# Kernel tuning notes

Measured on AMD Instinct MI355X. Metric: run time of the kernel, lower is better.

The kernel has to match this reference:

```python
import jax, jax.numpy as jnp
import numpy as np


def setup_inputs() -> dict:
    key = jax.random.key(0)
    ks = jax.random.split(key, 6)
    B, S, D, H, K = 16384, 16, 256, 128, 32
    s1 = 1.0 / np.sqrt(D)
    s2 = 1.0 / np.sqrt(H)
    s3 = 1.0 / np.sqrt(K)
    return {
        "x": jax.random.normal(ks[0], (B, D), jnp.float32),
        "W1": jax.random.normal(ks[1], (S, D, H), jnp.float32) * s1,
        "b1": jnp.zeros((S, H), jnp.float32),
        "W2": jax.random.normal(ks[2], (S, H, D), jnp.float32) * s2,
        "b2": jnp.zeros((S, D), jnp.float32),
        "Wc1": jax.random.normal(ks[3], (S, D, K), jnp.float32) * s1,
        "bc1": jnp.zeros((S, K), jnp.float32),
        "Wc2": jax.random.normal(ks[4], (S, K), jnp.float32) * s3,
        "bc2": jnp.zeros((S,), jnp.float32),
        "lam": jnp.ones((S,), jnp.float32) / S,  # lambda_weights init = 1/n_sources
    }


def reference(x, W1, b1, W2, b2, Wc1, bc1, Wc2, bc2, lam):
    # Batched per-source 2-layer MLP: [B,D] x [S,D,H] -> [B,S,H]
    h = jax.nn.relu(jnp.einsum("bd,sdh->bsh", x, W1) + b1[None])
    outs = jnp.einsum("bsh,shd->bsd", h, W2) + b2[None]            # [B,S,D]
    # Confidence net on each source output
    ch = jax.nn.relu(jnp.einsum("bsd,sdk->bsk", outs, Wc1) + bc1[None])
    conf = jax.nn.sigmoid(jnp.einsum("bsk,sk->bs", ch, Wc2) + bc2[None])  # [B,S]
    # Weighted, normalized combination
    cw = lam[None, :] * conf                                        # [B,S]
    cw = cw / (cw.sum(axis=1, keepdims=True) + 1e-6)
    out = jnp.einsum("bsd,bs->bd", outs, cw)                        # [B,D]
    return out
```

## Files before the change

### kernel.cpp

```cpp
#include <hip/hip_runtime.h>
#include <math.h>

#define S_N 16
#define D_N 256
#define H_N 128
#define K_N 32
#define BT  64
#define B_N 16384

typedef __attribute__((ext_vector_type(8))) short bf16x8;
typedef __attribute__((ext_vector_type(4))) float f32x4;
typedef __attribute__((ext_vector_type(16))) float f32x16;

#define MFMA16(a, b, c) __builtin_amdgcn_mfma_f32_16x16x32_bf16(a, b, c, 0, 0, 0)
#define MFMA32(a, b, c) __builtin_amdgcn_mfma_f32_32x32x16_bf16(a, b, c, 0, 0, 0)
#define SWZ(r) ((unsigned)(((r) & 15) << 4))

static __device__ __forceinline__ unsigned short f2bf(float f) {
  union { float f; unsigned u; } v; v.f = f;
  unsigned r = v.u + 0x7FFFu + ((v.u >> 16) & 1u);
  return (unsigned short)(r >> 16);
}

__global__ __launch_bounds__(256)
void lsi_prep(const float* __restrict__ W1, const float* __restrict__ W2,
              const float* __restrict__ Wc1, const float* __restrict__ b2,
              const float* __restrict__ bc1,
              unsigned short* __restrict__ W1t,
              unsigned short* __restrict__ W2t,
              unsigned short* __restrict__ Wft,
              float* __restrict__ bcf)
{
  const int bid = blockIdx.x;
  if (bid < 1024) {
    __shared__ float t[32][33];
    const float* src; unsigned short* dst; int R, C, r0, c0;
    if (bid < 512) {
      int s = bid >> 5, tt = bid & 31;
      R = 256; C = 128; r0 = (tt >> 2) * 32; c0 = (tt & 3) * 32;
      src = W1 + (size_t)s * 256 * 128; dst = W1t + (size_t)s * 128 * 256;
    } else {
      int s = (bid - 512) >> 5, tt = (bid - 512) & 31;
      R = 128; C = 256; r0 = (tt >> 3) * 32; c0 = (tt & 7) * 32;
      src = W2 + (size_t)s * 128 * 256; dst = W2t + (size_t)s * 256 * 128;
    }
    int li = threadIdx.x >> 5, lj = threadIdx.x & 31;
    #pragma unroll
    for (int i = 0; i < 4; ++i)
      t[li + i * 8][lj] = src[(size_t)(r0 + li + i * 8) * C + c0 + lj];
    __syncthreads();
    #pragma unroll
    for (int i = 0; i < 4; ++i)
      dst[(size_t)(c0 + li + i * 8) * R + r0 + lj] = f2bf(t[lj][li + i * 8]);
    return;
  }
  const int q  = bid - 1024;
  const int s  = q >> 3, hb = q & 7;
  const int t  = threadIdx.x;
  const int hh = hb * 16 + (t >> 4);
  const int kb = (t & 15) * 2;
  const float* w2r = W2 + ((size_t)s * H_N + hh) * D_N;
  const float* wc1 = Wc1 + (size_t)s * D_N * K_N;
  float a0 = 0.f, a1 = 0.f;
  for (int d = 0; d < D_N; ++d) {
    float wv = w2r[d];
    a0 = fmaf(wv, wc1[d * K_N + kb], a0);
    a1 = fmaf(wv, wc1[d * K_N + kb + 1], a1);
  }
  Wft[((size_t)s * K_N + kb) * H_N + hh]     = f2bf(a0);
  Wft[((size_t)s * K_N + kb + 1) * H_N + hh] = f2bf(a1);
  if (hb == 0 && t < K_N) {
    float a = bc1[s * K_N + t];
    for (int d = 0; d < D_N; ++d)
      a = fmaf(b2[s * D_N + d], wc1[d * K_N + t], a);
    bcf[s * K_N + t] = a;
  }
}

__global__ __launch_bounds__(512, 2)
void lsi_main(const float* __restrict__ x,
              const float* __restrict__ b1,
              const float* __restrict__ b2,
              const float* __restrict__ Wc2,
              const float* __restrict__ bc2,
              const float* __restrict__ lam,
              const unsigned short* __restrict__ W1t,
              const unsigned short* __restrict__ W2t,
              const unsigned short* __restrict__ Wft,
              const float* __restrict__ bcf,
              float* __restrict__ out)
{
  __shared__ unsigned short x_lds[BT * D_N];
  __shared__ unsigned short h_lds[2][BT * H_N];
  __shared__ float cw_lds[2][BT];
  __shared__ float wsum_lds[BT];

  const int tid = threadIdx.x;
  const int w   = tid >> 6;
  const int l   = tid & 63;
  const int l31 = l & 31;
  const int hi  = l >> 5;
  const int rA  = l & 15;
  const int g   = l >> 4;
  const int k8  = g * 8;
  const int b0  = blockIdx.x * BT;

  {
    int row = tid >> 3;
    int c0  = (tid & 7) * 32;
    const float* xr = x + (size_t)(b0 + row) * D_N + c0;
    #pragma unroll
    for (int cc = 0; cc < 4; ++cc) {
      float4 f0 = *(const float4*)(xr + cc * 8);
      float4 f1 = *(const float4*)(xr + cc * 8 + 4);
      bf16x8 u;
      u[0] = f2bf(f0.x); u[1] = f2bf(f0.y); u[2] = f2bf(f0.z); u[3] = f2bf(f0.w);
      u[4] = f2bf(f1.x); u[5] = f2bf(f1.y); u[6] = f2bf(f1.z); u[7] = f2bf(f1.w);
      unsigned off = (unsigned)(row * 512 + (c0 + cc * 8) * 2) ^ SWZ(row);
      *(bf16x8*)((char*)x_lds + off) = u;
    }
  }
  if (tid < BT) wsum_lds[tid] = 0.f;

  f32x16 out_acc[2];
  f32x16 acc2[2];
  #pragma unroll
  for (int i = 0; i < 16; ++i) { out_acc[0][i] = 0.f; out_acc[1][i] = 0.f; }

  auto do_gemm1 = [&](int s, unsigned short* hw) {
    const int rt1 = w >> 2, ct1 = w & 3;
    const int arow = rt1 * 32 + l31;
    const int hcol = ct1 * 32 + l31;
    f32x16 acc1;
    #pragma unroll
    for (int i = 0; i < 16; ++i) acc1[i] = 0.f;
    const unsigned short* B1 = W1t + ((size_t)s * H_N + hcol) * D_N + hi * 8;
    #pragma unroll
    for (int kf = 0; kf < 16; ++kf) {
      bf16x8 bfr = *(const bf16x8*)(B1 + kf * 16);
      unsigned off = (unsigned)(arow * 512 + kf * 32 + hi * 16) ^ SWZ(arow);
      bf16x8 afr = *(const bf16x8*)((const char*)x_lds + off);
      acc1 = MFMA32(afr, bfr, acc1);
    }
    const float b1v = b1[s * H_N + hcol];
    #pragma unroll
    for (int r = 0; r < 16; ++r) {
      int row = rt1 * 32 + (r & 3) + 8 * (r >> 2) + 4 * hi;
      float v = fmaxf(acc1[r] + b1v, 0.f);
      unsigned off = (unsigned)(row * 256 + hcol * 2) ^ SWZ(row);
      *(unsigned short*)((char*)hw + off) = f2bf(v);
    }
  };

  __syncthreads();
  do_gemm1(0, h_lds[0]);
  __syncthreads();

  for (int s = 0; s < S_N; ++s) {
    const unsigned short* hr = (const unsigned short*)h_lds[s & 1];

    if (s > 0) {
      #pragma unroll
      for (int rt = 0; rt < 2; ++rt)
        #pragma unroll
        for (int q = 0; q < 4; ++q) {
          f32x4 c4 = *(const f32x4*)&cw_lds[(s + 1) & 1][rt * 32 + q * 8 + hi * 4];
          #pragma unroll
          for (int i = 0; i < 4; ++i)
            out_acc[rt][q * 4 + i] += c4[i] * acc2[rt][q * 4 + i];
        }
    }

    if (w < 4) {
      f32x4 acc3[2];
      acc3[0] = (f32x4){0.f, 0.f, 0.f, 0.f};
      acc3[1] = (f32x4){0.f, 0.f, 0.f, 0.f};
      const unsigned short* Bf = Wft + ((size_t)s * K_N + rA) * H_N + k8;
      #pragma unroll
      for (int ks = 0; ks < 4; ++ks) {
        int row = w * 16 + rA;
        unsigned off = (unsigned)(row * 256 + (ks * 32 + k8) * 2) ^ SWZ(row);
        bf16x8 afr = *(const bf16x8*)((const char*)hr + off);
        acc3[0] = MFMA16(afr, *(const bf16x8*)(Bf + ks * 32), acc3[0]);
        acc3[1] = MFMA16(afr, *(const bf16x8*)(Bf + 16 * H_N + ks * 32), acc3[1]);
      }
      const float bcf0 = bcf[s * K_N + rA],  bcf1 = bcf[s * K_N + 16 + rA];
      const float wc20 = Wc2[s * K_N + rA],  wc21 = Wc2[s * K_N + 16 + rA];
      float pz[4];
      #pragma unroll
      for (int i = 0; i < 4; ++i)
        pz[i] = fmaxf(acc3[0][i] + bcf0, 0.f) * wc20 +
                fmaxf(acc3[1][i] + bcf1, 0.f) * wc21;
      #pragma unroll
      for (int m = 1; m < 16; m <<= 1)
        #pragma unroll
        for (int i = 0; i < 4; ++i)
          pz[i] += __shfl_xor(pz[i], m);
      if (rA == 0) {
        const float lam_s = lam[s], bc2_s = bc2[s];
        #pragma unroll
        for (int i = 0; i < 4; ++i) {
          float cv = lam_s / (1.f + __expf(-(pz[i] + bc2_s)));
          cw_lds[s & 1][w * 16 + g * 4 + i] = cv;
          wsum_lds[w * 16 + g * 4 + i] += cv;
        }
      }
    }

    #pragma unroll
    for (int i = 0; i < 16; ++i) { acc2[0][i] = 0.f; acc2[1][i] = 0.f; }
    {
      const int dcol = w * 32 + l31;
      const unsigned short* B2 = W2t + ((size_t)s * D_N + dcol) * H_N + hi * 8;
      #pragma unroll
      for (int kf = 0; kf < 8; ++kf) {
        bf16x8 bfr = *(const bf16x8*)(B2 + kf * 16);
        #pragma unroll
        for (int rt = 0; rt < 2; ++rt) {
          int arow = rt * 32 + l31;
          unsigned off = (unsigned)(arow * 256 + kf * 32 + hi * 16) ^ SWZ(arow);
          bf16x8 afr = *(const bf16x8*)((const char*)hr + off);
          acc2[rt] = MFMA32(afr, bfr, acc2[rt]);
        }
      }
      const float b2v = b2[s * D_N + dcol];
      #pragma unroll
      for (int rt = 0; rt < 2; ++rt)
        #pragma unroll
        for (int r = 0; r < 16; ++r)
          acc2[rt][r] += b2v;
    }

    if (s + 1 < S_N) do_gemm1(s + 1, h_lds[(s + 1) & 1]);

    __syncthreads();
  }

  #pragma unroll
  for (int rt = 0; rt < 2; ++rt)
    #pragma unroll
    for (int q = 0; q < 4; ++q) {
      f32x4 c4 = *(const f32x4*)&cw_lds[(S_N - 1) & 1][rt * 32 + q * 8 + hi * 4];
      #pragma unroll
      for (int i = 0; i < 4; ++i)
        out_acc[rt][q * 4 + i] += c4[i] * acc2[rt][q * 4 + i];
    }
  {
    const int dcol = w * 32 + l31;
    #pragma unroll
    for (int rt = 0; rt < 2; ++rt)
      #pragma unroll
      for (int q = 0; q < 4; ++q) {
        f32x4 w4 = *(const f32x4*)&wsum_lds[rt * 32 + q * 8 + hi * 4];
        #pragma unroll
        for (int i = 0; i < 4; ++i) {
          int row = rt * 32 + q * 8 + hi * 4 + i;
          float winv = 1.f / (w4[i] + 1e-6f);
          out[(size_t)(b0 + row) * D_N + dcol] = out_acc[rt][q * 4 + i] * winv;
        }
      }
  }
}

extern "C" void kernel_launch(void* const* d_in, const int* in_sizes, int n_in,
                              void* d_out, int out_size, void* d_ws, size_t ws_size,
                              hipStream_t stream) {
  const float* x   = (const float*)d_in[0];
  const float* W1  = (const float*)d_in[1];
  const float* b1  = (const float*)d_in[2];
  const float* W2  = (const float*)d_in[3];
  const float* b2  = (const float*)d_in[4];
  const float* Wc1 = (const float*)d_in[5];
  const float* bc1 = (const float*)d_in[6];
  const float* Wc2 = (const float*)d_in[7];
  const float* bc2 = (const float*)d_in[8];
  const float* lam = (const float*)d_in[9];
  float* out = (float*)d_out;

  unsigned short* W1t = (unsigned short*)d_ws;
  unsigned short* W2t = W1t + (size_t)S_N * H_N * D_N;
  unsigned short* Wft = W2t + (size_t)S_N * D_N * H_N;
  float* bcf = (float*)(Wft + (size_t)S_N * K_N * H_N);

  lsi_prep<<<dim3(1152), dim3(256), 0, stream>>>(W1, W2, Wc1, b2, bc1,
                                                 W1t, W2t, Wft, bcf);
  lsi_main<<<dim3(B_N / BT), dim3(512), 0, stream>>>(x, b1, b2, Wc2, bc2, lam,
                                                     W1t, W2t, Wft, bcf, out);
}
```

Baseline: 136.4 us.

## Transpose MFMA operand roles, reorder GEMM1 earlier, vectorize stores via LDS staging

Swaps the A/B operand roles in all MFMAs so each lane's accumulator covers batch rows along lanes and feature columns along registers. This turns the h writes into packed 4-element stores and lets the confidence reduction use two cross-lane shuffles instead of four rounds. GEMM1 for the next source now runs before the confidence and GEMM2 work, and uses two independent accumulator chains to expose more MFMA parallelism. The output is staged through LDS so global stores become coalesced 16-byte writes. In exchange it adds extra barriers at the end and more register pressure from the dual accumulators.

```diff
diff --git a/kernel.cpp b/kernel.cpp
--- a/kernel.cpp
+++ b/kernel.cpp
@@ -9,6 +9,7 @@
 #define B_N 16384
 
 typedef __attribute__((ext_vector_type(8))) short bf16x8;
+typedef __attribute__((ext_vector_type(4))) short bf16x4;
 typedef __attribute__((ext_vector_type(4))) float f32x4;
 typedef __attribute__((ext_vector_type(16))) float f32x16;
 
@@ -90,8 +91,8 @@
               const float* __restrict__ bcf,
               float* __restrict__ out)
 {
-  __shared__ unsigned short x_lds[BT * D_N];
-  __shared__ unsigned short h_lds[2][BT * H_N];
+  __shared__ __align__(16) unsigned short x_lds[BT * D_N];
+  __shared__ __align__(16) unsigned short h_lds[2][BT * H_N];
   __shared__ float cw_lds[2][BT];
   __shared__ float wsum_lds[BT];
 
@@ -100,10 +101,11 @@
   const int l   = tid & 63;
   const int l31 = l & 31;
   const int hi  = l >> 5;
-  const int rA  = l & 15;
+  const int l15 = l & 15;
   const int g   = l >> 4;
-  const int k8  = g * 8;
   const int b0  = blockIdx.x * BT;
+  const int bt1 = w >> 2;
+  const int ct1 = w & 3;
 
   {
     int row = tid >> 3;
@@ -122,33 +124,37 @@
   }
   if (tid < BT) wsum_lds[tid] = 0.f;
 
-  f32x16 out_acc[2];
-  f32x16 acc2[2];
+  f32x16 out_acc[2], acc2[2];
   #pragma unroll
-  for (int i = 0; i < 16; ++i) { out_acc[0][i] = 0.f; out_acc[1][i] = 0.f; }
+  for (int i = 0; i < 16; ++i) {
+    out_acc[0][i] = 0.f; out_acc[1][i] = 0.f;
+  }
 
   auto do_gemm1 = [&](int s, unsigned short* hw) {
-    const int rt1 = w >> 2, ct1 = w & 3;
-    const int arow = rt1 * 32 + l31;
-    const int hcol = ct1 * 32 + l31;
-    f32x16 acc1;
-    #pragma unroll
-    for (int i = 0; i < 16; ++i) acc1[i] = 0.f;
-    const unsigned short* B1 = W1t + ((size_t)s * H_N + hcol) * D_N + hi * 8;
-    #pragma unroll
-    for (int kf = 0; kf < 16; ++kf) {
-      bf16x8 bfr = *(const bf16x8*)(B1 + kf * 16);
-      unsigned off = (unsigned)(arow * 512 + kf * 32 + hi * 16) ^ SWZ(arow);
-      bf16x8 afr = *(const bf16x8*)((const char*)x_lds + off);
-      acc1 = MFMA32(afr, bfr, acc1);
-    }
-    const float b1v = b1[s * H_N + hcol];
-    #pragma unroll
-    for (int r = 0; r < 16; ++r) {
-      int row = rt1 * 32 + (r & 3) + 8 * (r >> 2) + 4 * hi;
-      float v = fmaxf(acc1[r] + b1v, 0.f);
-      unsigned off = (unsigned)(row * 256 + hcol * 2) ^ SWZ(row);
-      *(unsigned short*)((char*)hw + off) = f2bf(v);
+    const int brow = bt1 * 32 + l31;
+    f32x16 a1a, a1b;
+    #pragma unroll
+    for (int i = 0; i < 16; ++i) { a1a[i] = 0.f; a1b[i] = 0.f; }
+    const unsigned short* A1 = W1t + ((size_t)s * H_N + ct1 * 32 + l31) * D_N + hi * 8;
+    const unsigned xbase = (unsigned)(brow * 512 + hi * 16);
+    #pragma unroll
+    for (int kf = 0; kf < 16; kf += 2) {
+      bf16x8 aw0 = *(const bf16x8*)(A1 + kf * 16);
+      bf16x8 aw1 = *(const bf16x8*)(A1 + kf * 16 + 16);
+      bf16x8 bx0 = *(const bf16x8*)((const char*)x_lds + ((xbase + kf * 32) ^ SWZ(brow)));
+      bf16x8 bx1 = *(const bf16x8*)((const char*)x_lds + ((xbase + kf * 32 + 32) ^ SWZ(brow)));
+      a1a = MFMA32(aw0, bx0, a1a);
+      a1b = MFMA32(aw1, bx1, a1b);
+    }
+    #pragma unroll
+    for (int q = 0; q < 4; ++q) {
+      f32x4 b4 = *(const f32x4*)(b1 + s * H_N + ct1 * 32 + q * 8 + hi * 4);
+      bf16x4 hv;
+      #pragma unroll
+      for (int i = 0; i < 4; ++i)
+        hv[i] = (short)f2bf(fmaxf(a1a[q * 4 + i] + a1b[q * 4 + i] + b4[i], 0.f));
+      unsigned off = (unsigned)(brow * 256 + (ct1 * 32 + q * 8 + hi * 4) * 2) ^ SWZ(brow);
+      *(bf16x4*)((char*)hw + off) = hv;
     }
   };
 
@@ -160,105 +166,112 @@
     const unsigned short* hr = (const unsigned short*)h_lds[s & 1];
 
     if (s > 0) {
-      #pragma unroll
-      for (int rt = 0; rt < 2; ++rt)
-        #pragma unroll
-        for (int q = 0; q < 4; ++q) {
-          f32x4 c4 = *(const f32x4*)&cw_lds[(s + 1) & 1][rt * 32 + q * 8 + hi * 4];
-          #pragma unroll
-          for (int i = 0; i < 4; ++i)
-            out_acc[rt][q * 4 + i] += c4[i] * acc2[rt][q * 4 + i];
-        }
-    }
+      float cw0 = cw_lds[(s - 1) & 1][l31];
+      float cw1 = cw_lds[(s - 1) & 1][32 + l31];
+      #pragma unroll
+      for (int r = 0; r < 16; ++r) {
+        out_acc[0][r] += cw0 * acc2[0][r];
+        out_acc[1][r] += cw1 * acc2[1][r];
+      }
+    }
+
+    if (s + 1 < S_N) do_gemm1(s + 1, h_lds[(s + 1) & 1]);
 
     if (w < 4) {
-      f32x4 acc3[2];
-      acc3[0] = (f32x4){0.f, 0.f, 0.f, 0.f};
-      acc3[1] = (f32x4){0.f, 0.f, 0.f, 0.f};
-      const unsigned short* Bf = Wft + ((size_t)s * K_N + rA) * H_N + k8;
+      const int crow = w * 16 + l15;
+      f32x4 c3a = (f32x4){0.f, 0.f, 0.f, 0.f};
+      f32x4 c3b = (f32x4){0.f, 0.f, 0.f, 0.f};
+      const unsigned short* Af = Wft + ((size_t)s * K_N + l15) * H_N + g * 8;
+      const unsigned cb = (unsigned)(crow * 256 + g * 16);
       #pragma unroll
       for (int ks = 0; ks < 4; ++ks) {
-        int row = w * 16 + rA;
-        unsigned off = (unsigned)(row * 256 + (ks * 32 + k8) * 2) ^ SWZ(row);
-        bf16x8 afr = *(const bf16x8*)((const char*)hr + off);
-        acc3[0] = MFMA16(afr, *(const bf16x8*)(Bf + ks * 32), acc3[0]);
-        acc3[1] = MFMA16(afr, *(const bf16x8*)(Bf + 16 * H_N + ks * 32), acc3[1]);
-      }
-      const float bcf0 = bcf[s * K_N + rA],  bcf1 = bcf[s * K_N + 16 + rA];
-      const float wc20 = Wc2[s * K_N + rA],  wc21 = Wc2[s * K_N + 16 + rA];
-      float pz[4];
-      #pragma unroll
-      for (int i = 0; i < 4; ++i)
-        pz[i] = fmaxf(acc3[0][i] + bcf0, 0.f) * wc20 +
-                fmaxf(acc3[1][i] + bcf1, 0.f) * wc21;
-      #pragma unroll
-      for (int m = 1; m < 16; m <<= 1)
+        bf16x8 hb = *(const bf16x8*)((const char*)hr + ((cb + ks * 64) ^ SWZ(crow)));
+        c3a = MFMA16(*(const bf16x8*)(Af + ks * 32), hb, c3a);
+        c3b = MFMA16(*(const bf16x8*)(Af + 16 * H_N + ks * 32), hb, c3b);
+      }
+      float zz = 0.f;
+      {
+        f32x4 bcf4 = *(const f32x4*)(bcf + s * K_N + g * 4);
+        f32x4 wc4  = *(const f32x4*)(Wc2 + s * K_N + g * 4);
         #pragma unroll
         for (int i = 0; i < 4; ++i)
-          pz[i] += __shfl_xor(pz[i], m);
-      if (rA == 0) {
-        const float lam_s = lam[s], bc2_s = bc2[s];
+          zz += fmaxf(c3a[i] + bcf4[i], 0.f) * wc4[i];
+        bcf4 = *(const f32x4*)(bcf + s * K_N + 16 + g * 4);
+        wc4  = *(const f32x4*)(Wc2 + s * K_N + 16 + g * 4);
+        #pragma unroll
+        for (int i = 0; i < 4; ++i)
+          zz += fmaxf(c3b[i] + bcf4[i], 0.f) * wc4[i];
+      }
+      zz += __shfl_xor(zz, 16);
+      zz += __shfl_xor(zz, 32);
+      if (l < 16) {
+        float cv = lam[s] / (1.f + __expf(-(zz + bc2[s])));
+        cw_lds[s & 1][w * 16 + l] = cv;
+        wsum_lds[w * 16 + l] += cv;
+      }
+    }
+
+    #pragma unroll
+    for (int i = 0; i < 16; ++i) { acc2[0][i] = 0.f; acc2[1][i] = 0.f; }
+    {
+      const unsigned short* A2 = W2t + ((size_t)s * D_N + w * 32 + l31) * H_N + hi * 8;
+      const unsigned hb0 = (unsigned)(l31 * 256 + hi * 16);
+      const unsigned hb1 = (unsigned)((32 + l31) * 256 + hi * 16);
+      #pragma unroll
+      for (int kf = 0; kf < 8; ++kf) {
+        bf16x8 aw = *(const bf16x8*)(A2 + kf * 16);
+        bf16x8 h0 = *(const bf16x8*)((const char*)hr + ((hb0 + kf * 32) ^ SWZ(l31)));
+        bf16x8 h1 = *(const bf16x8*)((const char*)hr + ((hb1 + kf * 32) ^ SWZ(l31)));
+        acc2[0] = MFMA32(aw, h0, acc2[0]);
+        acc2[1] = MFMA32(aw, h1, acc2[1]);
+      }
+      #pragma unroll
+      for (int q = 0; q < 4; ++q) {
+        f32x4 b24 = *(const f32x4*)(b2 + s * D_N + w * 32 + q * 8 + hi * 4);
         #pragma unroll
         for (int i = 0; i < 4; ++i) {
-          float cv = lam_s / (1.f + __expf(-(pz[i] + bc2_s)));
-          cw_lds[s & 1][w * 16 + g * 4 + i] = cv;
-          wsum_lds[w * 16 + g * 4 + i] += cv;
+          acc2[0][q * 4 + i] += b24[i];
+          acc2[1][q * 4 + i] += b24[i];
         }
       }
     }
-
-    #pragma unroll
-    for (int i = 0; i < 16; ++i) { acc2[0][i] = 0.f; acc2[1][i] = 0.f; }
-    {
-      const int dcol = w * 32 + l31;
-      const unsigned short* B2 = W2t + ((size_t)s * D_N + dcol) * H_N + hi * 8;
-      #pragma unroll
-      for (int kf = 0; kf < 8; ++kf) {
-        bf16x8 bfr = *(const bf16x8*)(B2 + kf * 16);
+    __syncthreads();
+  }
+
+  {
+    float cw0 = cw_lds[(S_N - 1) & 1][l31];
+    float cw1 = cw_lds[(S_N - 1) & 1][32 + l31];
+    float wi0 = 1.f / (wsum_lds[l31] + 1e-6f);
+    float wi1 = 1.f / (wsum_lds[32 + l31] + 1e-6f);
+    #pragma unroll
+    for (int r = 0; r < 16; ++r) {
+      out_acc[0][r] = (out_acc[0][r] + cw0 * acc2[0][r]) * wi0;
+      out_acc[1][r] = (out_acc[1][r] + cw1 * acc2[1][r]) * wi1;
+    }
+  }
+  {
+    float* tb = (w < 4 ? (float*)x_lds : (float*)h_lds) + (w & 3) * 1152;
+    #pragma unroll
+    for (int t = 0; t < 2; ++t) {
+      __syncthreads();
+      #pragma unroll
+      for (int q = 0; q < 4; ++q) {
+        f32x4 v;
         #pragma unroll
-        for (int rt = 0; rt < 2; ++rt) {
-          int arow = rt * 32 + l31;
-          unsigned off = (unsigned)(arow * 256 + kf * 32 + hi * 16) ^ SWZ(arow);
-          bf16x8 afr = *(const bf16x8*)((const char*)hr + off);
-          acc2[rt] = MFMA32(afr, bfr, acc2[rt]);
-        }
-      }
-      const float b2v = b2[s * D_N + dcol];
-      #pragma unroll
-      for (int rt = 0; rt < 2; ++rt)
-        #pragma unroll
-        for (int r = 0; r < 16; ++r)
-          acc2[rt][r] += b2v;
-    }
-
-    if (s + 1 < S_N) do_gemm1(s + 1, h_lds[(s + 1) & 1]);
-
-    __syncthreads();
-  }
-
-  #pragma unroll
-  for (int rt = 0; rt < 2; ++rt)
-    #pragma unroll
-    for (int q = 0; q < 4; ++q) {
-      f32x4 c4 = *(const f32x4*)&cw_lds[(S_N - 1) & 1][rt * 32 + q * 8 + hi * 4];
-      #pragma unroll
-      for (int i = 0; i < 4; ++i)
-        out_acc[rt][q * 4 + i] += c4[i] * acc2[rt][q * 4 + i];
-    }
-  {
-    const int dcol = w * 32 + l31;
-    #pragma unroll
-    for (int rt = 0; rt < 2; ++rt)
-      #pragma unroll
-      for (int q = 0; q < 4; ++q) {
-        f32x4 w4 = *(const f32x4*)&wsum_lds[rt * 32 + q * 8 + hi * 4];
-        #pragma unroll
-        for (int i = 0; i < 4; ++i) {
-          int row = rt * 32 + q * 8 + hi * 4 + i;
-          float winv = 1.f / (w4[i] + 1e-6f);
-          out[(size_t)(b0 + row) * D_N + dcol] = out_acc[rt][q * 4 + i] * winv;
-        }
-      }
+        for (int i = 0; i < 4; ++i) v[i] = out_acc[t][q * 4 + i];
+        *(f32x4*)(tb + l31 * 36 + q * 8 + hi * 4) = v;
+      }
+      __syncthreads();
+      #pragma unroll
+      for (int p = 0; p < 2; ++p) {
+        int row = (l >> 2) + p * 16;
+        f32x4 v0 = *(const f32x4*)(tb + row * 36 + (l & 3) * 8);
+        f32x4 v1 = *(const f32x4*)(tb + row * 36 + (l & 3) * 8 + 4);
+        float* op = out + (size_t)(b0 + t * 32 + row) * D_N + w * 32 + (l & 3) * 8;
+        *(f32x4*)op = v0;
+        *(f32x4*)(op + 4) = v1;
+      }
+    }
   }
 }
 
```

Result: no change. 137.8 us (+1.0%).
